# Kernel tuning notes

Hardware: AMD Instinct MI355X
Metric: run time of the kernel (lower is better)

The kernel has to match this reference:

```python
import jax, jax.numpy as jnp
import numpy as np

B, C, H, W = 8, 96, 56, 56
N = H * W
K = 9
EPS = 1e-5

def _inorm(x):
    # InstanceNorm2d(affine=False): normalize over spatial dims per (batch, channel)
    m = jnp.mean(x, axis=(2, 3), keepdims=True)
    v = jnp.var(x, axis=(2, 3), keepdims=True)
    return (x - m) * jax.lax.rsqrt(v + EPS)

def _conv1(x, w, b):
    # 1x1 conv: (B,Cin,H,W) x (Cout,Cin) -> (B,Cout,H,W)
    return jnp.einsum('bchw,oc->bohw', x, w) + b[None, :, None, None]

def _grapher(x, rp, fc1_w, fc1_b, mr_w, mr_b, fc2_w, fc2_b):
    shortcut = x
    x = _inorm(_conv1(x, fc1_w, fc1_b))
    b, c, h, w = x.shape
    n = h * w
    xf = x.reshape(b, c, n)  # (B,C,N)
    # dynamic kNN on l2-normalized, gradient-stopped features (torch.no_grad + detach)
    xn = jax.lax.stop_gradient(xf)
    xn = xn / jnp.maximum(jnp.linalg.norm(xn, axis=1, keepdims=True), 1e-12)
    xt = jnp.swapaxes(xn, 1, 2)  # (B,N,C)
    sq = jnp.sum(xt * xt, axis=-1, keepdims=True)  # (B,N,1)
    dist = sq - 2.0 * jnp.einsum('bnc,bmc->bnm', xt, xt) + jnp.swapaxes(sq, 1, 2)
    dist = dist + rp  # relative_pos bias added to distances
    _, nn_idx = jax.lax.top_k(-dist, K)  # (B,N,K)
    # max-relative graph conv: gather neighbors, max over (x_j - x_i)
    x_j = jnp.take_along_axis(xf[:, :, None, :], nn_idx[:, None, :, :], axis=3)  # (B,C,N,K)
    xm = jnp.max(x_j - xf[:, :, :, None], axis=-1)  # (B,C,N)
    # channel-interleaved concat: (B,C,2,N,1) -> (B,2C,N,1)
    y = jnp.stack([xf, xm], axis=2).reshape(b, 2 * c, n, 1)
    y = jax.nn.gelu(_inorm(_conv1(y, mr_w, mr_b)), approximate=False)
    y = y.reshape(b, 2 * c, h, w)
    y = _inorm(_conv1(y, fc2_w, fc2_b))
    return y + shortcut

def _ffn(x, w1, b1, w2, b2):
    shortcut = x
    x = jax.nn.gelu(_inorm(_conv1(x, w1, b1)), approximate=False)
    x = _inorm(_conv1(x, w2, b2))
    return x + shortcut

_PARAM_SHAPES = [
    ('g1_fc1_w', (C, C)), ('g1_fc1_b', (C,)), ('g1_mr_w', (2*C, 2*C)), ('g1_mr_b', (2*C,)),
    ('g1_fc2_w', (C, 2*C)), ('g1_fc2_b', (C,)),
    ('g2_fc1_w', (C, C)), ('g2_fc1_b', (C,)), ('g2_mr_w', (2*C, 2*C)), ('g2_mr_b', (2*C,)),
    ('g2_fc2_w', (C, 2*C)), ('g2_fc2_b', (C,)),
    ('f1_fc1_w', (4*C, C)), ('f1_fc1_b', (4*C,)), ('f1_fc2_w', (C, 4*C)), ('f1_fc2_b', (C,)),
    ('f2_fc1_w', (4*C, C)), ('f2_fc1_b', (4*C,)), ('f2_fc2_w', (C, 4*C)), ('f2_fc2_b', (C,)),
]

def setup_inputs():
    key = jax.random.key(0)
    ks = jax.random.split(key, 2 + len(_PARAM_SHAPES))
    inp = {
        'x': jax.random.normal(ks[0], (B, C, H, W), dtype=jnp.float32),
        'relative_pos': jax.random.normal(ks[1], (1, N, N), dtype=jnp.float32) * 0.1,
    }
    for i, (nm, shp) in enumerate(_PARAM_SHAPES):
        inp[nm] = jax.random.normal(ks[i + 2], shp, dtype=jnp.float32) * 0.02
    return inp

def reference(x, relative_pos,
              g1_fc1_w, g1_fc1_b, g1_mr_w, g1_mr_b, g1_fc2_w, g1_fc2_b,
              g2_fc1_w, g2_fc1_b, g2_mr_w, g2_mr_b, g2_fc2_w, g2_fc2_b,
              f1_fc1_w, f1_fc1_b, f1_fc2_w, f1_fc2_b,
              f2_fc1_w, f2_fc1_b, f2_fc2_w, f2_fc2_b):
    y = _grapher(x, relative_pos, g1_fc1_w, g1_fc1_b, g1_mr_w, g1_mr_b, g1_fc2_w, g1_fc2_b)
    y = _ffn(y, f1_fc1_w, f1_fc1_b, f1_fc2_w, f1_fc2_b)
    y = jax.nn.relu(_inorm(y))
    y = _grapher(y, relative_pos, g2_fc1_w, g2_fc1_b, g2_mr_w, g2_mr_b, g2_fc2_w, g2_fc2_b)
    y = _ffn(y, f2_fc1_w, f2_fc1_b, f2_fc2_w, f2_fc2_b)
    y = _inorm(y)
    return x + y
```

## Files before the change

kernel.cpp:

```cpp
#include <hip/hip_runtime.h>
#include <math.h>

#define NN 3136
#define CC 96
#define BB 8
#define KNB 9
#define PARTS 7
#define FLT_MAX_ 3.402823466e+38f
typedef unsigned long long u64;
typedef unsigned short ushortT;
typedef __attribute__((ext_vector_type(8))) short short8;
typedef __attribute__((ext_vector_type(4))) float f32x4;

__global__ __launch_bounds__(256) void conv1_kernel(
    const float* __restrict__ in, const float* __restrict__ w,
    const float* __restrict__ bias, float* __restrict__ out, int K, int O)
{
    __shared__ float sW[16][64];
    __shared__ float sX[16][64];
    const int b  = blockIdx.z;
    const int n0 = blockIdx.x * 64;
    const int o0 = blockIdx.y * 64;
    const int tid = threadIdx.x;
    const int tx = tid & 15, ty = tid >> 4;
    const float* inb = in + (size_t)b * K * NN;

    float acc[4][4] = {{0.f}};

    for (int kb = 0; kb < K; kb += 16) {
        __syncthreads();
        {
            int o  = tid >> 2;
            int k4 = (tid & 3) << 2;
            float4 wv = make_float4(0.f, 0.f, 0.f, 0.f);
            if (o0 + o < O)
                wv = *(const float4*)&w[(size_t)(o0 + o) * K + kb + k4];
            sW[k4 + 0][o] = wv.x; sW[k4 + 1][o] = wv.y;
            sW[k4 + 2][o] = wv.z; sW[k4 + 3][o] = wv.w;
        }
        #pragma unroll
        for (int i = 0; i < 4; i++) {
            int e = tid + i * 256;
            int kk = e >> 6, n2 = e & 63;
            sX[kk][n2] = inb[(size_t)(kb + kk) * NN + n0 + n2];
        }
        __syncthreads();
        #pragma unroll
        for (int kk = 0; kk < 16; kk++) {
            const float4 av = *(const float4*)&sW[kk][ty << 2];
            const float4 xv = *(const float4*)&sX[kk][tx << 2];
            float a_[4] = {av.x, av.y, av.z, av.w};
            float x_[4] = {xv.x, xv.y, xv.z, xv.w};
            #pragma unroll
            for (int i = 0; i < 4; i++)
                #pragma unroll
                for (int j = 0; j < 4; j++)
                    acc[i][j] = fmaf(a_[i], x_[j], acc[i][j]);
        }
    }
    #pragma unroll
    for (int i = 0; i < 4; i++) {
        int o = o0 + (ty << 2) + i;
        if (o < O) {
            float bo = bias[o];
            float4 v = make_float4(acc[i][0] + bo, acc[i][1] + bo,
                                   acc[i][2] + bo, acc[i][3] + bo);
            *(float4*)&out[((size_t)b * O + o) * NN + n0 + (tx << 2)] = v;
        }
    }
}

__global__ __launch_bounds__(256) void inorm_kernel(
    const float* __restrict__ in, float* __restrict__ out,
    const float* __restrict__ res, int act)
{
    const int row = blockIdx.x;
    const float* x = in + (size_t)row * NN;
    const int tid = threadIdx.x;

    float v[13];
    float s = 0.f;
    #pragma unroll
    for (int i = 0; i < 13; i++) {
        int idx = tid + i * 256;
        v[i] = (idx < NN) ? x[idx] : 0.f;
        s += v[i];
    }
    __shared__ float red[4];
    #pragma unroll
    for (int off = 32; off > 0; off >>= 1) s += __shfl_down(s, off);
    if ((tid & 63) == 0) red[tid >> 6] = s;
    __syncthreads();
    const float mean = (red[0] + red[1] + red[2] + red[3]) * (1.f / (float)NN);

    float s2 = 0.f;
    #pragma unroll
    for (int i = 0; i < 13; i++) {
        int idx = tid + i * 256;
        if (idx < NN) { float d = v[i] - mean; s2 = fmaf(d, d, s2); }
    }
    #pragma unroll
    for (int off = 32; off > 0; off >>= 1) s2 += __shfl_down(s2, off);
    __syncthreads();
    if ((tid & 63) == 0) red[tid >> 6] = s2;
    __syncthreads();
    const float var = (red[0] + red[1] + red[2] + red[3]) * (1.f / (float)NN);
    const float rs = rsqrtf(var + 1e-5f);

    float* o = out + (size_t)row * NN;
    const float* rr = res ? (res + (size_t)row * NN) : nullptr;
    #pragma unroll
    for (int i = 0; i < 13; i++) {
        int idx = tid + i * 256;
        if (idx < NN) {
            float y = (v[i] - mean) * rs;
            if (act == 1)      y = 0.5f * y * (1.f + erff(y * 0.70710678118654752f));
            else if (act == 2) y = fmaxf(y, 0.f);
            if (rr) y += rr[idx];
            o[idx] = y;
        }
    }
}

__device__ __forceinline__ unsigned bf16rne(float x)
{
    unsigned u = __float_as_uint(x);
    return (u + 0x7fffu + ((u >> 16) & 1u)) >> 16;
}

__global__ __launch_bounds__(256) void colnorm_kernel(
    const float* __restrict__ xf, ushortT* __restrict__ xh,
    ushortT* __restrict__ xm, ushortT* __restrict__ xl,
    float* __restrict__ sqc)
{
    const int g = blockIdx.x * 256 + threadIdx.x;
    const int b = g / NN;
    const int n = g - b * NN;
    const float* p = xf + (size_t)b * CC * NN + n;

    float s = 0.f;
    for (int c = 0; c < CC; c++) { float t = p[(size_t)c * NN]; s = fmaf(t, t, s); }
    const float den = fmaxf(sqrtf(s), 1e-12f);

    const size_t o = (size_t)g * CC;
    float sq = 0.f;
    for (int c = 0; c < CC; c++) {
        float t = p[(size_t)c * NN] / den;
        sq = fmaf(t, t, sq);
        unsigned hr = bf16rne(t);
        float hf = __uint_as_float(hr << 16);
        float r1 = t - hf;
        unsigned mr = bf16rne(r1);
        float mf = __uint_as_float(mr << 16);
        float r2 = r1 - mf;
        unsigned lr = bf16rne(r2);
        xh[o + c] = (ushortT)hr;
        xm[o + c] = (ushortT)mr;
        xl[o + c] = (ushortT)lr;
    }
    sqc[g] = sq;
}

__device__ __forceinline__ u64 dkey(float d, int m)
{
    unsigned int ub = __float_as_uint(d);
    ub ^= (unsigned int)(((int)ub) >> 31) | 0x80000000u;
    return ((u64)ub << 32) | (unsigned int)m;
}
__device__ __forceinline__ void ins9u(u64 (&kk)[9], u64 key)
{
    if (key < kk[8]) {
        kk[8] = key;
        #pragma unroll
        for (int j = 8; j > 0; --j) {
            if (kk[j] < kk[j - 1]) {
                u64 t = kk[j]; kk[j] = kk[j - 1]; kk[j - 1] = t;
            }
        }
    }
}

__global__ __launch_bounds__(512, 4) void knn_mfma_kernel(
    const ushortT* __restrict__ xh, const ushortT* __restrict__ xm,
    const ushortT* __restrict__ xl, const float* __restrict__ sqc,
    const float* __restrict__ rp, u64* __restrict__ pko)
{
    __shared__ ushortT shA[3][64][104];
    __shared__ ushortT shB[3][32][104];
    __shared__ float   shD[64][33];
    const int b    = blockIdx.z;
    const int part = blockIdx.y;
    const int r0   = blockIdx.x * 64;
    const int tid  = threadIdx.x;
    const int ty = tid >> 3;
    const int tx = tid & 7;
    const int w  = tid >> 6;
    const int l  = tid & 63;
    const int Rt = w & 3;
    const int Mt = w >> 2;
    const int fr = l & 15;
    const int fq = l >> 4;
    const float* sqb = sqc + (size_t)b * NN;

    #pragma unroll
    for (int i = 0; i < 5; i++) {
        int idx = tid + i * 512;
        if (idx < 2304) {
            int s = idx / 768, rem = idx - s * 768;
            int r = rem / 12, cc = (rem - r * 12) * 8;
            const ushortT* bp = (s == 0) ? xh : ((s == 1) ? xm : xl);
            *(float4*)&shA[s][r][cc] =
                *(const float4*)&bp[((size_t)(b * NN + r0 + r)) * CC + cc];
        }
    }

    u64 kk0[9];
    #pragma unroll
    for (int j = 0; j < 9; j++) kk0[j] = 0xFFFFFFFFFFFFFFFFull;

    for (int mt = 0; mt < 14; mt++) {
        const int m0 = part * 448 + mt * 32;

        #pragma unroll
        for (int i = 0; i < 3; i++) {
            int idx = tid + i * 512;
            if (idx < 1152) {
                int s = idx / 384, rem = idx - s * 384;
                int m = rem / 12, cc = (rem - m * 12) * 8;
                const ushortT* bp = (s == 0) ? xh : ((s == 1) ? xm : xl);
                *(float4*)&shB[s][m][cc] =
                    *(const float4*)&bp[((size_t)(b * NN + m0 + m)) * CC + cc];
            }
        }
        const float4 sqv = *(const float4*)&sqb[m0 + tx * 4];
        const float4 rpv = *(const float4*)&rp[(size_t)(r0 + ty) * NN + m0 + tx * 4];
        __syncthreads();

        f32x4 acc = {0.f, 0.f, 0.f, 0.f};
        #pragma unroll
        for (int kc = 0; kc < 3; kc++) {
            const int ca = kc * 32 + fq * 8;
            const short8 ah = *(const short8*)&shA[0][Rt * 16 + fr][ca];
            const short8 am = *(const short8*)&shA[1][Rt * 16 + fr][ca];
            const short8 al = *(const short8*)&shA[2][Rt * 16 + fr][ca];
            const short8 bh = *(const short8*)&shB[0][Mt * 16 + fr][ca];
            const short8 bm = *(const short8*)&shB[1][Mt * 16 + fr][ca];
            const short8 bl = *(const short8*)&shB[2][Mt * 16 + fr][ca];
            acc = __builtin_amdgcn_mfma_f32_16x16x32_bf16(ah, bh, acc, 0, 0, 0);
            acc = __builtin_amdgcn_mfma_f32_16x16x32_bf16(ah, bm, acc, 0, 0, 0);
            acc = __builtin_amdgcn_mfma_f32_16x16x32_bf16(am, bh, acc, 0, 0, 0);
            acc = __builtin_amdgcn_mfma_f32_16x16x32_bf16(am, bm, acc, 0, 0, 0);
            acc = __builtin_amdgcn_mfma_f32_16x16x32_bf16(ah, bl, acc, 0, 0, 0);
            acc = __builtin_amdgcn_mfma_f32_16x16x32_bf16(al, bh, acc, 0, 0, 0);
        }
        #pragma unroll
        for (int q = 0; q < 4; q++)
            shD[Rt * 16 + fq * 4 + q][Mt * 16 + fr] = acc[q];
        __syncthreads();

        const float d0 = shD[ty][tx * 4 + 0];
        const float d1 = shD[ty][tx * 4 + 1];
        const float d2 = shD[ty][tx * 4 + 2];
        const float d3 = shD[ty][tx * 4 + 3];
        const int mb = m0 + tx * 4;
        ins9u(kk0, dkey(fmaf(-2.f, d0, sqv.x + rpv.x), mb + 0));
        ins9u(kk0, dkey(fmaf(-2.f, d1, sqv.y + rpv.y), mb + 1));
        ins9u(kk0, dkey(fmaf(-2.f, d2, sqv.z + rpv.z), mb + 2));
        ins9u(kk0, dkey(fmaf(-2.f, d3, sqv.w + rpv.w), mb + 3));
    }

    const size_t base = ((size_t)(b * NN + r0 + ty) * PARTS + part) * KNB;
    #pragma unroll
    for (int k = 0; k < 9; k++) {
        u64 wv = kk0[0];
        #pragma unroll
        for (int off = 1; off < 8; off <<= 1) {
            unsigned int lo = __shfl_xor((unsigned int)wv, off);
            unsigned int hi = __shfl_xor((unsigned int)(wv >> 32), off);
            u64 o = ((u64)hi << 32) | lo;
            wv = (o < wv) ? o : wv;
        }
        if (kk0[0] == wv) {
            #pragma unroll
            for (int j = 0; j < 8; j++) kk0[j] = kk0[j + 1];
            kk0[8] = 0xFFFFFFFFFFFFFFFFull;
        }
        if (tx == 0) pko[base + k] = wv;
    }
}

__global__ __launch_bounds__(256) void knn_merge_kernel(
    const u64* __restrict__ pko, int* __restrict__ nn_idx)
{
    const int g = blockIdx.x * 256 + threadIdx.x;
    if (g >= BB * NN) return;
    u64 kk[9];
    #pragma unroll
    for (int j = 0; j < 9; j++) kk[j] = 0xFFFFFFFFFFFFFFFFull;
    const u64* v = pko + (size_t)g * PARTS * KNB;
    for (int p = 0; p < PARTS; p++)
        #pragma unroll
        for (int j = 0; j < 9; j++)
            ins9u(kk, v[p * KNB + j]);
    #pragma unroll
    for (int j = 0; j < 9; j++)
        nn_idx[(size_t)g * KNB + j] = (int)(kk[j] & 0xFFFFFFFFu);
}

__global__ __launch_bounds__(256) void gather_kernel(
    const float* __restrict__ xf, const int* __restrict__ nn_idx,
    float* __restrict__ y)
{
    const size_t g = (size_t)blockIdx.x * 256 + threadIdx.x;
    const int n  = (int)(g % NN);
    const int bc = (int)(g / NN);
    const int c  = bc % CC;
    const int b  = bc / CC;
    const float* row = xf + (size_t)(b * CC + c) * NN;
    const float xi = row[n];
    const int* id = nn_idx + ((size_t)b * NN + n) * KNB;
    float mx = -FLT_MAX_;
    #pragma unroll
    for (int k = 0; k < KNB; k++) mx = fmaxf(mx, row[id[k]] - xi);
    float* o = y + ((size_t)b * 2 * CC + 2 * c) * NN + n;
    o[0]  = xi;
    o[NN] = mx;
}

static void conv1(const float* in, const float* w, const float* b, float* out,
                  int K, int O, hipStream_t s)
{
    dim3 grid(NN / 64, (O + 63) / 64, BB);
    conv1_kernel<<<grid, 256, 0, s>>>(in, w, b, out, K, O);
}
static void inorm(const float* in, float* out, const float* res, int ch, int act,
                  hipStream_t s)
{
    inorm_kernel<<<BB * ch, 256, 0, s>>>(in, out, res, act);
}

struct GrapherP {
    const float *fc1w, *fc1b, *mrw, *mrb, *fc2w, *fc2b;
};

static void run_grapher(const float* in, const float* rp, const GrapherP& p,
                        float* outCur, float* bufA, float* bufB,
                        ushortT* xh, ushortT* xm, ushortT* xl,
                        float* sqc, int* idx, hipStream_t s)
{
    conv1(in, p.fc1w, p.fc1b, bufA, CC, CC, s);
    inorm(bufA, bufB, nullptr, CC, 0, s);
    colnorm_kernel<<<(BB * NN) / 256, 256, 0, s>>>(bufB, xh, xm, xl, sqc);
    u64* pko = (u64*)bufA;
    knn_mfma_kernel<<<dim3(NN / 64, PARTS, BB), 512, 0, s>>>(
        xh, xm, xl, sqc, rp, pko);
    knn_merge_kernel<<<(BB * NN + 255) / 256, 256, 0, s>>>(pko, idx);
    gather_kernel<<<(BB * CC * NN) / 256, 256, 0, s>>>(bufB, idx, bufA);
    conv1(bufA, p.mrw, p.mrb, bufB, 2 * CC, 2 * CC, s);
    inorm(bufB, bufA, nullptr, 2 * CC, 1, s);
    conv1(bufA, p.fc2w, p.fc2b, bufB, 2 * CC, CC, s);
    inorm(bufB, outCur, in, CC, 0, s);
}

static void run_ffn(const float* in, const float* w1, const float* b1,
                    const float* w2, const float* b2,
                    float* outCur, float* bufA, float* bufB, hipStream_t s)
{
    conv1(in, w1, b1, bufA, CC, 4 * CC, s);
    inorm(bufA, bufB, nullptr, 4 * CC, 1, s);
    conv1(bufB, w2, b2, bufA, 2 * CC * 2, CC, s);
    inorm(bufA, outCur, in, CC, 0, s);
}

extern "C" void kernel_launch(void* const* d_in, const int* in_sizes, int n_in,
                              void* d_out, int out_size, void* d_ws, size_t ws_size,
                              hipStream_t stream)
{
    const float* x  = (const float*)d_in[0];
    const float* rp = (const float*)d_in[1];
    GrapherP g1 = {(const float*)d_in[2],  (const float*)d_in[3],
                   (const float*)d_in[4],  (const float*)d_in[5],
                   (const float*)d_in[6],  (const float*)d_in[7]};
    GrapherP g2 = {(const float*)d_in[8],  (const float*)d_in[9],
                   (const float*)d_in[10], (const float*)d_in[11],
                   (const float*)d_in[12], (const float*)d_in[13]};
    const float* f1w1 = (const float*)d_in[14]; const float* f1b1 = (const float*)d_in[15];
    const float* f1w2 = (const float*)d_in[16]; const float* f1b2 = (const float*)d_in[17];
    const float* f2w1 = (const float*)d_in[18]; const float* f2b1 = (const float*)d_in[19];
    const float* f2w2 = (const float*)d_in[20]; const float* f2b2 = (const float*)d_in[21];
    float* out = (float*)d_out;

    const size_t P  = (size_t)BB * CC * NN;
    const size_t P4 = 4 * P;
    float* ws   = (float*)d_ws;
    float* bufA = ws;
    float* bufB = bufA + P4;
    float* cur0 = bufB + P4;
    float* cur1 = cur0 + P;
    float* sqc  = cur1 + P;
    int*   idx  = (int*)(sqc + (size_t)BB * NN);
    ushortT* xh = (ushortT*)(idx + (size_t)BB * NN * KNB);
    ushortT* xm = xh + P;
    ushortT* xl = xm + P;

    run_grapher(x, rp, g1, cur0, bufA, bufB, xh, xm, xl, sqc, idx, stream);
    run_ffn(cur0, f1w1, f1b1, f1w2, f1b2, cur1, bufA, bufB, stream);
    inorm(cur1, cur0, nullptr, CC, 2, stream);
    run_grapher(cur0, rp, g2, cur1, bufA, bufB, xh, xm, xl, sqc, idx, stream);
    run_ffn(cur1, f2w1, f2b1, f2w2, f2b2, cur0, bufA, bufB, stream);
    inorm(cur0, out, x, CC, 0, stream);
    (void)in_sizes; (void)n_in; (void)out_size; (void)ws_size;
}
```

Baseline: 1.160 ms.

## Hold kNN A-tile fragments in registers and prefetch next B tile early

The kNN MFMA kernel now loads each wave's A-operand fragments (hi/mid/lo bf16 splits) straight from global memory into registers once, replacing the shared-memory A tile and its per-iteration LDS reads. The B tile for the next column block is loaded into shared memory right after the second barrier, before the top-k insertion work, so the load can overlap the selection code. This cuts LDS traffic and shared-memory footprint, which could allow more resident blocks. The cost is extra registers for the nine short8 fragments, and it depends on the existing barrier order to keep shB reuse safe.

```diff
diff --git a/kernel.cpp b/kernel.cpp
--- a/kernel.cpp
+++ b/kernel.cpp
@@ -185,7 +185,6 @@
     const ushortT* __restrict__ xl, const float* __restrict__ sqc,
     const float* __restrict__ rp, u64* __restrict__ pko)
 {
-    __shared__ ushortT shA[3][64][104];
     __shared__ ushortT shB[3][32][104];
     __shared__ float   shD[64][33];
     const int b    = blockIdx.z;
@@ -202,25 +201,24 @@
     const int fq = l >> 4;
     const float* sqb = sqc + (size_t)b * NN;
 
-    #pragma unroll
-    for (int i = 0; i < 5; i++) {
-        int idx = tid + i * 512;
-        if (idx < 2304) {
-            int s = idx / 768, rem = idx - s * 768;
-            int r = rem / 12, cc = (rem - r * 12) * 8;
-            const ushortT* bp = (s == 0) ? xh : ((s == 1) ? xm : xl);
-            *(float4*)&shA[s][r][cc] =
-                *(const float4*)&bp[((size_t)(b * NN + r0 + r)) * CC + cc];
-        }
-    }
+    const size_t arow = ((size_t)(b * NN + r0 + Rt * 16 + fr)) * CC;
+    const int ko = fq * 8;
+    const short8 ah0 = *(const short8*)&xh[arow + ko];
+    const short8 ah1 = *(const short8*)&xh[arow + 32 + ko];
+    const short8 ah2 = *(const short8*)&xh[arow + 64 + ko];
+    const short8 am0 = *(const short8*)&xm[arow + ko];
+    const short8 am1 = *(const short8*)&xm[arow + 32 + ko];
+    const short8 am2 = *(const short8*)&xm[arow + 64 + ko];
+    const short8 al0 = *(const short8*)&xl[arow + ko];
+    const short8 al1 = *(const short8*)&xl[arow + 32 + ko];
+    const short8 al2 = *(const short8*)&xl[arow + 64 + ko];
 
     u64 kk0[9];
     #pragma unroll
     for (int j = 0; j < 9; j++) kk0[j] = 0xFFFFFFFFFFFFFFFFull;
 
-    for (int mt = 0; mt < 14; mt++) {
-        const int m0 = part * 448 + mt * 32;
-
+    {
+        const int m0 = part * 448;
         #pragma unroll
         for (int i = 0; i < 3; i++) {
             int idx = tid + i * 512;
@@ -232,31 +230,71 @@
                     *(const float4*)&bp[((size_t)(b * NN + m0 + m)) * CC + cc];
             }
         }
+    }
+
+    for (int mt = 0; mt < 14; mt++) {
+        const int m0 = part * 448 + mt * 32;
+
         const float4 sqv = *(const float4*)&sqb[m0 + tx * 4];
         const float4 rpv = *(const float4*)&rp[(size_t)(r0 + ty) * NN + m0 + tx * 4];
         __syncthreads();
 
         f32x4 acc = {0.f, 0.f, 0.f, 0.f};
-        #pragma unroll
-        for (int kc = 0; kc < 3; kc++) {
-            const int ca = kc * 32 + fq * 8;
-            const short8 ah = *(const short8*)&shA[0][Rt * 16 + fr][ca];
-            const short8 am = *(const short8*)&shA[1][Rt * 16 + fr][ca];
-            const short8 al = *(const short8*)&shA[2][Rt * 16 + fr][ca];
+        {
+            const int ca = fq * 8;
             const short8 bh = *(const short8*)&shB[0][Mt * 16 + fr][ca];
             const short8 bm = *(const short8*)&shB[1][Mt * 16 + fr][ca];
             const short8 bl = *(const short8*)&shB[2][Mt * 16 + fr][ca];
-            acc = __builtin_amdgcn_mfma_f32_16x16x32_bf16(ah, bh, acc, 0, 0, 0);
-            acc = __builtin_amdgcn_mfma_f32_16x16x32_bf16(ah, bm, acc, 0, 0, 0);
-            acc = __builtin_amdgcn_mfma_f32_16x16x32_bf16(am, bh, acc, 0, 0, 0);
-            acc = __builtin_amdgcn_mfma_f32_16x16x32_bf16(am, bm, acc, 0, 0, 0);
-            acc = __builtin_amdgcn_mfma_f32_16x16x32_bf16(ah, bl, acc, 0, 0, 0);
-            acc = __builtin_amdgcn_mfma_f32_16x16x32_bf16(al, bh, acc, 0, 0, 0);
+            acc = __builtin_amdgcn_mfma_f32_16x16x32_bf16(ah0, bh, acc, 0, 0, 0);
+            acc = __builtin_amdgcn_mfma_f32_16x16x32_bf16(ah0, bm, acc, 0, 0, 0);
+            acc = __builtin_amdgcn_mfma_f32_16x16x32_bf16(am0, bh, acc, 0, 0, 0);
+            acc = __builtin_amdgcn_mfma_f32_16x16x32_bf16(am0, bm, acc, 0, 0, 0);
+            acc = __builtin_amdgcn_mfma_f32_16x16x32_bf16(ah0, bl, acc, 0, 0, 0);
+            acc = __builtin_amdgcn_mfma_f32_16x16x32_bf16(al0, bh, acc, 0, 0, 0);
+        }
+        {
+            const int ca = 32 + fq * 8;
+            const short8 bh = *(const short8*)&shB[0][Mt * 16 + fr][ca];
+            const short8 bm = *(const short8*)&shB[1][Mt * 16 + fr][ca];
+            const short8 bl = *(const short8*)&shB[2][Mt * 16 + fr][ca];
+            acc = __builtin_amdgcn_mfma_f32_16x16x32_bf16(ah1, bh, acc, 0, 0, 0);
+            acc = __builtin_amdgcn_mfma_f32_16x16x32_bf16(ah1, bm, acc, 0, 0, 0);
+            acc = __builtin_amdgcn_mfma_f32_16x16x32_bf16(am1, bh, acc, 0, 0, 0);
+            acc = __builtin_amdgcn_mfma_f32_16x16x32_bf16(am1, bm, acc, 0, 0, 0);
+            acc = __builtin_amdgcn_mfma_f32_16x16x32_bf16(ah1, bl, acc, 0, 0, 0);
+            acc = __builtin_amdgcn_mfma_f32_16x16x32_bf16(al1, bh, acc, 0, 0, 0);
+        }
+        {
+            const int ca = 64 + fq * 8;
+            const short8 bh = *(const short8*)&shB[0][Mt * 16 + fr][ca];
+            const short8 bm = *(const short8*)&shB[1][Mt * 16 + fr][ca];
+            const short8 bl = *(const short8*)&shB[2][Mt * 16 + fr][ca];
+            acc = __builtin_amdgcn_mfma_f32_16x16x32_bf16(ah2, bh, acc, 0, 0, 0);
+            acc = __builtin_amdgcn_mfma_f32_16x16x32_bf16(ah2, bm, acc, 0, 0, 0);
+            acc = __builtin_amdgcn_mfma_f32_16x16x32_bf16(am2, bh, acc, 0, 0, 0);
+            acc = __builtin_amdgcn_mfma_f32_16x16x32_bf16(am2, bm, acc, 0, 0, 0);
+            acc = __builtin_amdgcn_mfma_f32_16x16x32_bf16(ah2, bl, acc, 0, 0, 0);
+            acc = __builtin_amdgcn_mfma_f32_16x16x32_bf16(al2, bh, acc, 0, 0, 0);
         }
         #pragma unroll
         for (int q = 0; q < 4; q++)
             shD[Rt * 16 + fq * 4 + q][Mt * 16 + fr] = acc[q];
         __syncthreads();
+
+        if (mt + 1 < 14) {
+            const int m0n = m0 + 32;
+            #pragma unroll
+            for (int i = 0; i < 3; i++) {
+                int idx = tid + i * 512;
+                if (idx < 1152) {
+                    int s = idx / 384, rem = idx - s * 384;
+                    int m = rem / 12, cc = (rem - m * 12) * 8;
+                    const ushortT* bp = (s == 0) ? xh : ((s == 1) ? xm : xl);
+                    *(float4*)&shB[s][m][cc] =
+                        *(const float4*)&bp[((size_t)(b * NN + m0n + m)) * CC + cc];
+                }
+            }
+        }
 
         const float d0 = shD[ty][tx * 4 + 0];
         const float d1 = shD[ty][tx * 4 + 1];
```

Measured after the change: 1.099 ms. 5.2% less time.

## Keep kNN A-fragments in registers, double-buffer B tiles, skip LDS distance staging

Applied to the files above, without the earlier changes.

The kNN MFMA kernel now loads each wave's query-row fragments (hi/mid/lo bf16 splits) straight from global memory into registers once, instead of staging them in shared memory. Candidate tiles are double-buffered in LDS, with the next tile's global loads issued before the current tile's MFMAs, so there is one barrier per tile instead of two. The MFMA operands are swapped so each lane holds four distances for its own row, which removes the shD round-trip. Per-lane top-9 lists are reduced across quad lanes with shuffles. Each wave-column (Mt) now writes its own partial list, so the merge kernel consumes twice as many partial lists. That requires the partial-result buffer to be twice as large and adds merge work.

```diff
diff --git a/kernel.cpp b/kernel.cpp
--- a/kernel.cpp
+++ b/kernel.cpp
@@ -185,15 +185,11 @@
     const ushortT* __restrict__ xl, const float* __restrict__ sqc,
     const float* __restrict__ rp, u64* __restrict__ pko)
 {
-    __shared__ ushortT shA[3][64][104];
-    __shared__ ushortT shB[3][32][104];
-    __shared__ float   shD[64][33];
+    __shared__ ushortT shB[2][3][32][104];
     const int b    = blockIdx.z;
     const int part = blockIdx.y;
     const int r0   = blockIdx.x * 64;
     const int tid  = threadIdx.x;
-    const int ty = tid >> 3;
-    const int tx = tid & 7;
     const int w  = tid >> 6;
     const int l  = tid & 63;
     const int Rt = w & 3;
@@ -202,79 +198,121 @@
     const int fq = l >> 4;
     const float* sqb = sqc + (size_t)b * NN;
 
-    #pragma unroll
-    for (int i = 0; i < 5; i++) {
-        int idx = tid + i * 512;
-        if (idx < 2304) {
-            int s = idx / 768, rem = idx - s * 768;
-            int r = rem / 12, cc = (rem - r * 12) * 8;
-            const ushortT* bp = (s == 0) ? xh : ((s == 1) ? xm : xl);
-            *(float4*)&shA[s][r][cc] =
-                *(const float4*)&bp[((size_t)(b * NN + r0 + r)) * CC + cc];
-        }
-    }
+    const int r = r0 + Rt * 16 + fr;
+    const size_t arow = ((size_t)(b * NN + r)) * CC;
+    const int ko = fq * 8;
+    const short8 ah0 = *(const short8*)&xh[arow + ko];
+    const short8 ah1 = *(const short8*)&xh[arow + 32 + ko];
+    const short8 ah2 = *(const short8*)&xh[arow + 64 + ko];
+    const short8 am0 = *(const short8*)&xm[arow + ko];
+    const short8 am1 = *(const short8*)&xm[arow + 32 + ko];
+    const short8 am2 = *(const short8*)&xm[arow + 64 + ko];
+    const short8 al0 = *(const short8*)&xl[arow + ko];
+    const short8 al1 = *(const short8*)&xl[arow + 32 + ko];
+    const short8 al2 = *(const short8*)&xl[arow + 64 + ko];
+
+    const int i0 = tid,        s0 = i0 / 384, re0 = i0 - s0 * 384;
+    const int m_0 = re0 / 12,  c_0 = (re0 - m_0 * 12) * 8;
+    const int i1 = tid + 512,  s1 = i1 / 384, re1 = i1 - s1 * 384;
+    const int m_1 = re1 / 12,  c_1 = (re1 - m_1 * 12) * 8;
+    const int i2 = tid + 1024, s2 = i2 / 384, re2 = i2 - s2 * 384;
+    const int m_2 = re2 / 12,  c_2 = (re2 - m_2 * 12) * 8;
+    const bool has2 = (tid < 128);
+    const ushortT* bp0 = (s0 == 0) ? xh : ((s0 == 1) ? xm : xl);
+    const ushortT* bp1 = (s1 == 0) ? xh : ((s1 == 1) ? xm : xl);
+    const ushortT* bp2 = (s2 == 0) ? xh : ((s2 == 1) ? xm : xl);
 
     u64 kk0[9];
     #pragma unroll
     for (int j = 0; j < 9; j++) kk0[j] = 0xFFFFFFFFFFFFFFFFull;
 
+    {
+        const int m0 = part * 448;
+        *(float4*)&shB[0][s0][m_0][c_0] =
+            *(const float4*)&bp0[((size_t)(b * NN + m0 + m_0)) * CC + c_0];
+        *(float4*)&shB[0][s1][m_1][c_1] =
+            *(const float4*)&bp1[((size_t)(b * NN + m0 + m_1)) * CC + c_1];
+        if (has2)
+            *(float4*)&shB[0][s2][m_2][c_2] =
+                *(const float4*)&bp2[((size_t)(b * NN + m0 + m_2)) * CC + c_2];
+    }
+
+    const int mloc = Mt * 16 + fq * 4;
+
     for (int mt = 0; mt < 14; mt++) {
-        const int m0 = part * 448 + mt * 32;
-
-        #pragma unroll
-        for (int i = 0; i < 3; i++) {
-            int idx = tid + i * 512;
-            if (idx < 1152) {
-                int s = idx / 384, rem = idx - s * 384;
-                int m = rem / 12, cc = (rem - m * 12) * 8;
-                const ushortT* bp = (s == 0) ? xh : ((s == 1) ? xm : xl);
-                *(float4*)&shB[s][m][cc] =
-                    *(const float4*)&bp[((size_t)(b * NN + m0 + m)) * CC + cc];
-            }
-        }
-        const float4 sqv = *(const float4*)&sqb[m0 + tx * 4];
-        const float4 rpv = *(const float4*)&rp[(size_t)(r0 + ty) * NN + m0 + tx * 4];
+        const int m0  = part * 448 + mt * 32;
+        const int cur = mt & 1;
+
+        float4 nxA, nxB, nxC;
+        const bool hasn = (mt + 1) < 14;
+        if (hasn) {
+            const int m0n = m0 + 32;
+            nxA = *(const float4*)&bp0[((size_t)(b * NN + m0n + m_0)) * CC + c_0];
+            nxB = *(const float4*)&bp1[((size_t)(b * NN + m0n + m_1)) * CC + c_1];
+            if (has2)
+                nxC = *(const float4*)&bp2[((size_t)(b * NN + m0n + m_2)) * CC + c_2];
+        }
+        const float4 sqv = *(const float4*)&sqb[m0 + mloc];
+        const float4 rpv = *(const float4*)&rp[(size_t)r * NN + m0 + mloc];
+
         __syncthreads();
 
         f32x4 acc = {0.f, 0.f, 0.f, 0.f};
-        #pragma unroll
-        for (int kc = 0; kc < 3; kc++) {
-            const int ca = kc * 32 + fq * 8;
-            const short8 ah = *(const short8*)&shA[0][Rt * 16 + fr][ca];
-            const short8 am = *(const short8*)&shA[1][Rt * 16 + fr][ca];
-            const short8 al = *(const short8*)&shA[2][Rt * 16 + fr][ca];
-            const short8 bh = *(const short8*)&shB[0][Mt * 16 + fr][ca];
-            const short8 bm = *(const short8*)&shB[1][Mt * 16 + fr][ca];
-            const short8 bl = *(const short8*)&shB[2][Mt * 16 + fr][ca];
-            acc = __builtin_amdgcn_mfma_f32_16x16x32_bf16(ah, bh, acc, 0, 0, 0);
-            acc = __builtin_amdgcn_mfma_f32_16x16x32_bf16(ah, bm, acc, 0, 0, 0);
-            acc = __builtin_amdgcn_mfma_f32_16x16x32_bf16(am, bh, acc, 0, 0, 0);
-            acc = __builtin_amdgcn_mfma_f32_16x16x32_bf16(am, bm, acc, 0, 0, 0);
-            acc = __builtin_amdgcn_mfma_f32_16x16x32_bf16(ah, bl, acc, 0, 0, 0);
-            acc = __builtin_amdgcn_mfma_f32_16x16x32_bf16(al, bh, acc, 0, 0, 0);
-        }
-        #pragma unroll
-        for (int q = 0; q < 4; q++)
-            shD[Rt * 16 + fq * 4 + q][Mt * 16 + fr] = acc[q];
-        __syncthreads();
-
-        const float d0 = shD[ty][tx * 4 + 0];
-        const float d1 = shD[ty][tx * 4 + 1];
-        const float d2 = shD[ty][tx * 4 + 2];
-        const float d3 = shD[ty][tx * 4 + 3];
-        const int mb = m0 + tx * 4;
-        ins9u(kk0, dkey(fmaf(-2.f, d0, sqv.x + rpv.x), mb + 0));
-        ins9u(kk0, dkey(fmaf(-2.f, d1, sqv.y + rpv.y), mb + 1));
-        ins9u(kk0, dkey(fmaf(-2.f, d2, sqv.z + rpv.z), mb + 2));
-        ins9u(kk0, dkey(fmaf(-2.f, d3, sqv.w + rpv.w), mb + 3));
-    }
-
-    const size_t base = ((size_t)(b * NN + r0 + ty) * PARTS + part) * KNB;
+        {
+            const short8 bh = *(const short8*)&shB[cur][0][Mt * 16 + fr][ko];
+            const short8 bm = *(const short8*)&shB[cur][1][Mt * 16 + fr][ko];
+            const short8 bl = *(const short8*)&shB[cur][2][Mt * 16 + fr][ko];
+            acc = __builtin_amdgcn_mfma_f32_16x16x32_bf16(bh, ah0, acc, 0, 0, 0);
+            acc = __builtin_amdgcn_mfma_f32_16x16x32_bf16(bh, am0, acc, 0, 0, 0);
+            acc = __builtin_amdgcn_mfma_f32_16x16x32_bf16(bm, ah0, acc, 0, 0, 0);
+            acc = __builtin_amdgcn_mfma_f32_16x16x32_bf16(bm, am0, acc, 0, 0, 0);
+            acc = __builtin_amdgcn_mfma_f32_16x16x32_bf16(bh, al0, acc, 0, 0, 0);
+            acc = __builtin_amdgcn_mfma_f32_16x16x32_bf16(bl, ah0, acc, 0, 0, 0);
+        }
+        {
+            const short8 bh = *(const short8*)&shB[cur][0][Mt * 16 + fr][32 + ko];
+            const short8 bm = *(const short8*)&shB[cur][1][Mt * 16 + fr][32 + ko];
+            const short8 bl = *(const short8*)&shB[cur][2][Mt * 16 + fr][32 + ko];
+            acc = __builtin_amdgcn_mfma_f32_16x16x32_bf16(bh, ah1, acc, 0, 0, 0);
+            acc = __builtin_amdgcn_mfma_f32_16x16x32_bf16(bh, am1, acc, 0, 0, 0);
+            acc = __builtin_amdgcn_mfma_f32_16x16x32_bf16(bm, ah1, acc, 0, 0, 0);
+            acc = __builtin_amdgcn_mfma_f32_16x16x32_bf16(bm, am1, acc, 0, 0, 0);
+            acc = __builtin_amdgcn_mfma_f32_16x16x32_bf16(bh, al1, acc, 0, 0, 0);
+            acc = __builtin_amdgcn_mfma_f32_16x16x32_bf16(bl, ah1, acc, 0, 0, 0);
+        }
+        {
+            const short8 bh = *(const short8*)&shB[cur][0][Mt * 16 + fr][64 + ko];
+            const short8 bm = *(const short8*)&shB[cur][1][Mt * 16 + fr][64 + ko];
+            const short8 bl = *(const short8*)&shB[cur][2][Mt * 16 + fr][64 + ko];
+            acc = __builtin_amdgcn_mfma_f32_16x16x32_bf16(bh, ah2, acc, 0, 0, 0);
+            acc = __builtin_amdgcn_mfma_f32_16x16x32_bf16(bh, am2, acc, 0, 0, 0);
+            acc = __builtin_amdgcn_mfma_f32_16x16x32_bf16(bm, ah2, acc, 0, 0, 0);
+            acc = __builtin_amdgcn_mfma_f32_16x16x32_bf16(bm, am2, acc, 0, 0, 0);
+            acc = __builtin_amdgcn_mfma_f32_16x16x32_bf16(bh, al2, acc, 0, 0, 0);
+            acc = __builtin_amdgcn_mfma_f32_16x16x32_bf16(bl, ah2, acc, 0, 0, 0);
+        }
+
+        if (hasn) {
+            const int nb = cur ^ 1;
+            *(float4*)&shB[nb][s0][m_0][c_0] = nxA;
+            *(float4*)&shB[nb][s1][m_1][c_1] = nxB;
+            if (has2) *(float4*)&shB[nb][s2][m_2][c_2] = nxC;
+        }
+
+        const int mb = m0 + mloc;
+        ins9u(kk0, dkey(fmaf(-2.f, acc[0], sqv.x + rpv.x), mb + 0));
+        ins9u(kk0, dkey(fmaf(-2.f, acc[1], sqv.y + rpv.y), mb + 1));
+        ins9u(kk0, dkey(fmaf(-2.f, acc[2], sqv.z + rpv.z), mb + 2));
+        ins9u(kk0, dkey(fmaf(-2.f, acc[3], sqv.w + rpv.w), mb + 3));
+    }
+
+    const size_t base =
+        (((size_t)(b * NN + r) * PARTS + part) * 2 + Mt) * KNB;
     #pragma unroll
     for (int k = 0; k < 9; k++) {
         u64 wv = kk0[0];
         #pragma unroll
-        for (int off = 1; off < 8; off <<= 1) {
+        for (int off = 16; off < 64; off <<= 1) {
             unsigned int lo = __shfl_xor((unsigned int)wv, off);
             unsigned int hi = __shfl_xor((unsigned int)(wv >> 32), off);
             u64 o = ((u64)hi << 32) | lo;
@@ -285,7 +323,7 @@
             for (int j = 0; j < 8; j++) kk0[j] = kk0[j + 1];
             kk0[8] = 0xFFFFFFFFFFFFFFFFull;
         }
-        if (tx == 0) pko[base + k] = wv;
+        if (fq == 0) pko[base + k] = wv;
     }
 }
 
@@ -297,8 +335,8 @@
     u64 kk[9];
     #pragma unroll
     for (int j = 0; j < 9; j++) kk[j] = 0xFFFFFFFFFFFFFFFFull;
-    const u64* v = pko + (size_t)g * PARTS * KNB;
-    for (int p = 0; p < PARTS; p++)
+    const u64* v = pko + (size_t)g * PARTS * 2 * KNB;
+    for (int p = 0; p < PARTS * 2; p++)
         #pragma unroll
         for (int j = 0; j < 9; j++)
             ins9u(kk, v[p * KNB + j]);
```

After: 1.109 ms. 4.4% less time.
